# Kernel optimization log

Measured on AMD Instinct MI355X. Metric: run time of the kernel, lower is better.

The kernel has to match this reference:

```python
import jax, jax.numpy as jnp
import numpy as np
from jax import lax

B, C_IN, H, W = 4, 64, 128, 128
NUM_HIDDEN = 64
KSIZE = 3
DIST = 1
MOVES = 2 * DIST + 1          # 3
MOVESQ = MOVES * MOVES        # 9
TIME_STEPS = 8
LOSS_WEIGHT = 0.01


def _shift(a, dy, dx):
    """out(y, x) = a(y+dy, x+dx), zero outside; dy,dx in {-1,0,1}. a: [..., H, W]."""
    p = jnp.pad(a, [(0, 0)] * (a.ndim - 2) + [(1, 1), (1, 1)])
    h, w = a.shape[-2], a.shape[-1]
    return p[..., 1 + dy:1 + dy + h, 1 + dx:1 + dx + w]


def _gather(o4):
    # gather_kernel[i,0,i//3,i%3]=1 => channel i is o4 shifted by (i//3-1, i%3-1)
    return jnp.stack([_shift(o4, i // MOVES - 1, i % MOVES - 1) for i in range(MOVESQ)], axis=1)


def _merge(hxo):
    # hxo: [B, nh, 9, H, W]; merge_kernel[0, 9-i-1, i//3, i%3]=1 grouped per hidden channel
    # => merged(y,x) = sum_j hxo[:,:,j](y + 1 - j//3, x + 1 - j%3)
    return sum(_shift(hxo[:, :, j], 1 - j // MOVES, 1 - j % MOVES) for j in range(MOVESQ))


def _forward(x, mask, w_ih, b_ih, w_hh, b_hh, w_ho, b_ho):
    b, _, h, w = x.shape
    pad = KSIZE // 2
    i_all = lax.conv_general_dilated(
        x, w_ih, (1, 1), [(pad, pad), (pad, pad)],
        dimension_numbers=("NCHW", "OIHW", "NCHW")) + b_ih[None, :, None, None]
    i_r, i_i, i_n = jnp.split(i_all, 3, axis=1)

    h0 = jnp.zeros((b, NUM_HIDDEN, h, w), x.dtype)
    loss0 = jnp.zeros((b, MOVESQ, h, w), x.dtype)  # scalar init broadcasts to this shape

    def step(carry, _):
        hid, loss = carry
        hh = jnp.einsum("bchw,oc->bohw", hid, w_hh) + b_hh[None, :, None, None]
        h_r, h_i, h_n = jnp.split(hh, 3, axis=1)
        resetgate = jax.nn.sigmoid(i_r + h_r)
        inputgate = jax.nn.sigmoid(i_i + h_i)
        newgate = jnp.tanh(i_n + resetgate * h_n)
        hy = newgate + inputgate * (hid - newgate)
        o = jax.nn.softmax(jnp.einsum("bchw,oc->bohw", hy, w_ho) + b_ho[None, :, None, None], axis=1)
        o4 = o[:, 4]
        diff = (_gather(o4) - o) ** 2 * o
        bce = -jnp.mean(mask * jnp.log(1.0 - o4) + (1.0 - mask) * jnp.log(o4))
        loss = loss + bce + diff * LOSS_WEIGHT
        hxo = jnp.einsum("bchw,bdhw->bcdhw", hy, o)  # [B, nh, 9, H, W]
        h_next = _merge(hxo)
        return (h_next, loss), (h_next, o)

    (_, loss), (hiddens, outs) = lax.scan(step, (h0, loss0), None, length=TIME_STEPS)
    return hiddens, outs, loss


def setup_inputs() -> dict:
    key = jax.random.key(0)
    ks = jax.random.split(key, 8)
    s = 0.05
    return {
        "x": jax.random.normal(ks[0], (B, C_IN, H, W), jnp.float32),
        "mask": jax.random.uniform(ks[1], (B, H, W), jnp.float32),
        "w_ih": jax.random.normal(ks[2], (3 * NUM_HIDDEN, C_IN, KSIZE, KSIZE), jnp.float32) * s,
        "b_ih": jax.random.normal(ks[3], (3 * NUM_HIDDEN,), jnp.float32) * s,
        "w_hh": jax.random.normal(ks[4], (3 * NUM_HIDDEN, NUM_HIDDEN), jnp.float32) * s,
        "b_hh": jax.random.normal(ks[5], (3 * NUM_HIDDEN,), jnp.float32) * s,
        "w_ho": jax.random.normal(ks[6], (MOVESQ, NUM_HIDDEN), jnp.float32) * s,
        "b_ho": jax.random.normal(ks[7], (MOVESQ,), jnp.float32) * s,
    }


def reference(x, mask, w_ih, b_ih, w_hh, b_hh, w_ho, b_ho):
    return _forward(x, mask, w_ih, b_ih, w_hh, b_hh, w_ho, b_ho)
```

## Files before the change

### kernel.cpp

```cpp
#include <hip/hip_runtime.h>

#define NP 16384
#define HID_SZ 4194304
#define O_SZ   589824
#define OUTS_OFF 33554432
#define LOSS_OFF 38273024

#define WS_IALL0 0
#define WS_IALL1 4194304
#define WS_XTH   6291456
#define WS_HYA   8388608
#define WS_HYB   10485776
#define WS_WHH   12582944
#define WS_WHOB  12589088
#define WS_BTF   12589600
#define WS_BCEP  12644896

typedef __attribute__((ext_vector_type(8))) short bf16x8;
typedef __attribute__((ext_vector_type(8))) unsigned short ushort8;
typedef __attribute__((ext_vector_type(4))) unsigned short usht4;
typedef __attribute__((ext_vector_type(4))) float f32x4;

__device__ __forceinline__ float frcp(float x) { return __builtin_amdgcn_rcpf(x); }
__device__ __forceinline__ unsigned short f2bf(float f) {
    unsigned int u = __float_as_uint(f);
    return (unsigned short)((u + 0x7fffu + ((u >> 16) & 1u)) >> 16);
}
__device__ __forceinline__ float bf2f(unsigned short h) {
    return __uint_as_float(((unsigned int)h) << 16);
}
__device__ __forceinline__ int swz_bid(int bid) { return ((bid & 7) << 7) | (bid >> 3); }

__global__ __launch_bounds__(256) void prep_all(const float* __restrict__ x,
                                                const float* __restrict__ w_hh,
                                                const float* __restrict__ w_ho,
                                                const float* __restrict__ w_ih,
                                                unsigned short* __restrict__ xTh,
                                                unsigned short* __restrict__ whhBf,
                                                unsigned short* __restrict__ whoBf,
                                                unsigned short* __restrict__ BTf) {
    const int tid = threadIdx.x;
    if (blockIdx.x < 256) {
        const int p = blockIdx.x * 256 + tid;
        const int b = p >> 14, yx = p & 16383;
        const size_t base = ((size_t)p) << 6;
        for (int ic0 = 0; ic0 < 64; ic0 += 8) {
            ushort8 vh;
#pragma unroll
            for (int j = 0; j < 8; ++j)
                vh[j] = f2bf(x[(((size_t)(b * 64 + ic0 + j)) << 14) + yx]);
            *(ushort8*)(xTh + base + ic0) = vh;
        }
    } else {
        int i = (blockIdx.x - 256) * 256 + tid;
        if (i < 12288) {
            int f = i >> 9, r = i & 511;
            int lane = r >> 3, e = r & 7, lrow = lane & 15, lkq = lane >> 4;
            int ih = f / 12, n = f % 12;
            whhBf[i] = f2bf(w_hh[(n * 16 + lrow) * 64 + ih * 32 + lkq * 8 + e]);
        } else if (i < 13312) {
            int j = i - 12288;
            int f = j >> 9, r = j & 511;
            int lane = r >> 3, e = r & 7, lrow = lane & 15, lkq = lane >> 4;
            whoBf[j] = (lrow < 9) ? f2bf(w_ho[lrow * 64 + f * 32 + lkq * 8 + e]) : (unsigned short)0;
        } else if (i < 13312 + 110592) {
            int k2 = i - 13312;
            int f = k2 >> 9, r = k2 & 511;
            int lane = r >> 3, e = r & 7, lrow = lane & 15, lkq = lane >> 4;
            int tapih = f / 12, n = f % 12;
            int tap = tapih >> 1, ih = tapih & 1;
            int oc = n * 16 + lrow, ic = ih * 32 + lkq * 8 + e;
            BTf[k2] = f2bf(w_ih[(oc * 64 + ic) * 9 + tap]);
        }
    }
}

__global__ __launch_bounds__(256, 4) void conv_step0(const unsigned short* __restrict__ xTh,
                                                     const unsigned short* __restrict__ BTf,
                                                     const float* __restrict__ b_ih,
                                                     const float* __restrict__ b_hh,
                                                     const unsigned short* __restrict__ whoBf,
                                                     const float* __restrict__ b_ho,
                                                     const float* __restrict__ mask,
                                                     unsigned short* __restrict__ iall0,
                                                     unsigned short* __restrict__ iall1,
                                                     unsigned short* __restrict__ hy_cur,
                                                     float* __restrict__ o_out,
                                                     float* __restrict__ bceP) {
    __shared__ __align__(16) unsigned char smem[25344];
    unsigned short* hy_p = (unsigned short*)(smem + 10656);
    float* red = (float*)(smem + 19872);
    const int tid = threadIdx.x;
    const int bid = swz_bid(blockIdx.x);
    const int b = bid >> 8, y = (bid >> 1) & 127, hh2 = bid & 1;
    const int pxb = hh2 * 64, yxrow = y * 128;

    for (int ch = tid; ch < 1584; ch += 256) {
        const int row = ch / 528;
        const int rem = ch - row * 528;
        const int pxl = rem >> 3, icc = rem & 7;
        const int gy = y + row - 1, gx = pxb + pxl - 1;
        ushort8 vh = {};
        if (gy >= 0 && gy < 128 && gx >= 0 && gx < 128) {
            const size_t go = ((size_t)(b * 16384 + gy * 128 + gx)) * 64 + icc * 8;
            vh = *(const ushort8*)(xTh + go);
        }
        const int off = ((row * 66 + pxl) * 128 + icc * 16) ^ ((pxl & 7) << 4);
        *(ushort8*)(smem + off) = vh;
    }
    __syncthreads();

    const int lane = tid & 63, wv = tid >> 6;
    const int lrow = lane & 15, lkq = lane >> 4;
    const unsigned short* BTl = BTf + lane * 8;

    f32x4 acc[12] = {};
#pragma unroll
    for (int tap = 0; tap < 9; ++tap) {
        const int row = tap / 3, dx = tap % 3 - 1;
#pragma unroll
        for (int ih = 0; ih < 2; ++ih) {
            const int pxl = wv * 16 + lrow + dx + 1;
            const int off = ((row * 66 + pxl) * 128 + ih * 64 + lkq * 16) ^ ((pxl & 7) << 4);
            bf16x8 Ah = *(const bf16x8*)(smem + off);
#pragma unroll
            for (int n = 0; n < 12; ++n) {
                bf16x8 Bh = *(const bf16x8*)(BTl + (((tap * 2 + ih) * 12 + n) << 9));
                acc[n] = __builtin_amdgcn_mfma_f32_16x16x32_bf16(Ah, Bh, acc[n], 0, 0, 0);
            }
        }
    }

    float bias[12];
#pragma unroll
    for (int n = 0; n < 12; ++n) bias[n] = b_ih[n * 16 + lrow];
    const size_t rowb = (size_t)((b * 128 + y) * 2 + hh2);
    ushort8 v0[4];
    usht4 v1[4];
#pragma unroll
    for (int r = 0; r < 4; ++r) {
#pragma unroll
        for (int n = 0; n < 8; ++n) v0[r][n] = f2bf(acc[n][r] + bias[n]);
#pragma unroll
        for (int n = 8; n < 12; ++n) v1[r][n - 8] = f2bf(acc[n][r] + bias[n]);
        *(ushort8*)(iall0 + (rowb << 13) + ((wv * 4 + r) << 9) + lane * 8) = v0[r];
        *(usht4*)(iall1 + (rowb << 12) + ((wv * 4 + r) << 8) + lane * 4) = v1[r];
    }
    __syncthreads();

    float bhr[4], bhi[4], bhn[4];
#pragma unroll
    for (int nf = 0; nf < 4; ++nf) {
        bhr[nf] = b_hh[nf * 16 + lrow];
        bhi[nf] = b_hh[64 + nf * 16 + lrow];
        bhn[nf] = b_hh[128 + nf * 16 + lrow];
    }
#pragma unroll
    for (int nf = 0; nf < 4; ++nf) {
        const int g = nf * 16 + lrow;
        usht4 hv4;
#pragma unroll
        for (int rr = 0; rr < 4; ++rr) {
            const int pxl = wv * 16 + lkq * 4 + rr;
            float ir = bf2f(v0[rr][nf]), ii = bf2f(v0[rr][4 + nf]), inn = bf2f(v1[rr][nf]);
            float rg = frcp(1.0f + __expf(-(ir + bhr[nf])));
            float ig = frcp(1.0f + __expf(-(ii + bhi[nf])));
            float t2 = __expf(2.0f * (inn + rg * bhn[nf]));
            float nn = 1.0f - 2.0f * frcp(t2 + 1.0f);
            unsigned short hv = f2bf(nn + ig * (0.0f - nn));
            hy_p[pxl * 72 + g] = hv;
            hv4[rr] = hv;
        }
        *(usht4*)(hy_cur + (((size_t)(b * 64 + g)) << 14) + yxrow + pxb + wv * 16 + lkq * 4) = hv4;
    }
    __syncthreads();

    f32x4 aco = {};
#pragma unroll
    for (int ih = 0; ih < 2; ++ih) {
        const int pxa = wv * 16 + lrow;
        bf16x8 Ao = *(const bf16x8*)(hy_p + pxa * 72 + ih * 32 + lkq * 8);
        bf16x8 Bo = *(const bf16x8*)(whoBf + ((ih << 9) + lane * 8));
        aco = __builtin_amdgcn_mfma_f32_16x16x32_bf16(Ao, Bo, aco, 0, 0, 0);
    }
    const float bho = (lrow < 9) ? b_ho[lrow] : 0.0f;
    float ov[4];
    float vbce = 0.0f;
    const int yx0 = yxrow + pxb + wv * 16 + lkq * 4;
#pragma unroll
    for (int r = 0; r < 4; ++r) {
        float lg = aco[r] + bho;
        float v = (lrow < 9) ? lg : -1e30f;
        v = fmaxf(v, __shfl_xor(v, 1));
        v = fmaxf(v, __shfl_xor(v, 2));
        v = fmaxf(v, __shfl_xor(v, 4));
        v = fmaxf(v, __shfl_xor(v, 8));
        float e = (lrow < 9) ? __expf(lg - v) : 0.0f;
        float s = e;
        s += __shfl_xor(s, 1);
        s += __shfl_xor(s, 2);
        s += __shfl_xor(s, 4);
        s += __shfl_xor(s, 8);
        ov[r] = e * frcp(s);
    }
    if (lrow < 9) {
        f32x4 wvec = {ov[0], ov[1], ov[2], ov[3]};
        *(f32x4*)(o_out + (((size_t)(b * 9 + lrow)) << 14) + yx0) = wvec;
    }
    if (lrow == 4) {
        const f32x4 mk = *(const f32x4*)(mask + (((size_t)b) << 14) + yx0);
#pragma unroll
        for (int r = 0; r < 4; ++r)
            vbce += mk[r] * __logf(1.0f - ov[r]) + (1.0f - mk[r]) * __logf(ov[r]);
    }
    float v = (lrow == 4) ? vbce : 0.0f;
#pragma unroll
    for (int d = 1; d < 64; d <<= 1) v += __shfl_xor(v, d);
    if (lane == 0) red[wv] = v;
    __syncthreads();
    if (tid == 0) bceP[bid] = red[0] + red[1] + red[2] + red[3];
}

__global__ __launch_bounds__(256, 4) void step_kernel(const unsigned short* __restrict__ hyp,
                                                      const float* __restrict__ o_prev,
                                                      const unsigned short* __restrict__ iall0,
                                                      const unsigned short* __restrict__ iall1,
                                                      const unsigned short* __restrict__ whhBf,
                                                      const float* __restrict__ b_hh,
                                                      const unsigned short* __restrict__ whoBf,
                                                      const float* __restrict__ b_ho,
                                                      const float* __restrict__ mask,
                                                      float* __restrict__ hidd_out,
                                                      unsigned short* __restrict__ hy_cur,
                                                      float* __restrict__ o_out,
                                                      float* __restrict__ bceP) {
    __shared__ __align__(16) unsigned char smem[19904];
    float* ostrip = (float*)(smem + 8192);
    unsigned short* hy_p = (unsigned short*)(smem + 10656);
    float* red = (float*)(smem + 19872);

    const int tid = threadIdx.x;
    const int bid = swz_bid(blockIdx.x);
    const int b = bid >> 8, y = (bid >> 1) & 127, hh2 = bid & 1;
    const int pxb = hh2 * 64, yxrow = y * 128;

    {
        const int c = tid >> 2, pq = tid & 3;
        const int gx0 = pxb + pq * 16;
        const unsigned short* hb = hyp + (((size_t)(b * 64 + c)) << 14);
        ushort8 w8[3][4];
#pragma unroll
        for (int r = 0; r < 3; ++r) {
            const int gyc = min(max(y + r - 1, 0), 127);
            const unsigned short* src = hb + gyc * 128 + gx0 - 8;
#pragma unroll
            for (int q = 0; q < 4; ++q) w8[r][q] = *(const ushort8*)(src + q * 8);
        }
        const float* ob = o_prev + (((size_t)b * 9) << 14);
        for (int e = tid; e < 594; e += 256) {
            const int j = e / 66, s = e - j * 66;
            const int rj = y + 1 - j / 3;
            const int gx = pxb - 1 + s;
            const bool ok = (rj >= 0) && (rj < 128) && (gx >= 0) && (gx < 128);
            ostrip[j * 68 + s] = ok ? ob[(((size_t)j) << 14) + rj * 128 + gx] : 0.0f;
        }
        __syncthreads();

        float a[16];
#pragma unroll
        for (int px = 0; px < 16; ++px) a[px] = 0.0f;
#pragma unroll
        for (int r = 0; r < 3; ++r) {
            float wf[18];
#pragma unroll
            for (int k = 0; k < 18; ++k)
                wf[k] = bf2f((unsigned short)w8[r][(k + 7) >> 3][(k + 7) & 7]);
#pragma unroll
            for (int ex = -1; ex <= 1; ++ex) {
                const int idx = r * 3 + (ex + 1);
                const int j = 8 - idx;
                const float* osj = ostrip + j * 68 + pq * 16 + 1 + ex;
#pragma unroll
                for (int px = 0; px < 16; ++px)
                    a[px] = fmaf(wf[px + ex + 1], osj[px], a[px]);
            }
        }
        const size_t hob = (((size_t)(b * 64 + c)) << 14) + yxrow + gx0;
#pragma unroll
        for (int q = 0; q < 4; ++q) {
            f32x4 v = {a[q * 4], a[q * 4 + 1], a[q * 4 + 2], a[q * 4 + 3]};
            *(f32x4*)(hidd_out + hob + q * 4) = v;
        }
#pragma unroll
        for (int px = 0; px < 16; ++px) {
            const int pxl = pq * 16 + px;
            *(unsigned short*)(smem + ((pxl * 128 + c * 2) ^ ((pxl & 7) << 4))) = f2bf(a[px]);
        }
        __syncthreads();
    }

    const int lane = tid & 63, wv = tid >> 6;
    const int lrow = lane & 15, lkq = lane >> 4;

    f32x4 acc[12] = {};
    {
        bf16x8 Ah[2];
#pragma unroll
        for (int ih = 0; ih < 2; ++ih) {
            const int pxa = wv * 16 + lrow;
            const int off = (pxa * 128 + ih * 64 + lkq * 16) ^ ((pxa & 7) << 4);
            Ah[ih] = *(const bf16x8*)(smem + off);
        }
#pragma unroll
        for (int ih = 0; ih < 2; ++ih)
#pragma unroll
            for (int n = 0; n < 12; ++n) {
                bf16x8 Bh = *(const bf16x8*)(whhBf + (((ih * 12 + n) << 9) + lane * 8));
                acc[n] = __builtin_amdgcn_mfma_f32_16x16x32_bf16(Ah[ih], Bh, acc[n], 0, 0, 0);
            }
    }

    float bhr[4], bhi[4], bhn[4];
#pragma unroll
    for (int nf = 0; nf < 4; ++nf) {
        bhr[nf] = b_hh[nf * 16 + lrow];
        bhi[nf] = b_hh[64 + nf * 16 + lrow];
        bhn[nf] = b_hh[128 + nf * 16 + lrow];
    }
    const size_t rowb = (size_t)((b * 128 + y) * 2 + hh2);
    const unsigned short* p0 = iall0 + (rowb << 13) + (wv << 11) + lane * 8;
    const unsigned short* p1 = iall1 + (rowb << 12) + (wv << 10) + lane * 4;
    ushort8 lo[4];
    usht4 hi[4];
#pragma unroll
    for (int rr = 0; rr < 4; ++rr) {
        lo[rr] = *(const ushort8*)(p0 + (rr << 9));
        hi[rr] = *(const usht4*)(p1 + (rr << 8));
    }
#pragma unroll
    for (int nf = 0; nf < 4; ++nf) {
        const int g = nf * 16 + lrow;
        usht4 hv4;
#pragma unroll
        for (int rr = 0; rr < 4; ++rr) {
            const int pxl = wv * 16 + lkq * 4 + rr;
            float hr = bhr[nf] + acc[nf][rr];
            float hig = bhi[nf] + acc[nf + 4][rr];
            float hn = bhn[nf] + acc[nf + 8][rr];
            float ir = bf2f(lo[rr][nf]), ii = bf2f(lo[rr][4 + nf]), inn = bf2f(hi[rr][nf]);
            float rg = frcp(1.0f + __expf(-(ir + hr)));
            float ig = frcp(1.0f + __expf(-(ii + hig)));
            float t2 = __expf(2.0f * (inn + rg * hn));
            float nn = 1.0f - 2.0f * frcp(t2 + 1.0f);
            const int offA = (pxl * 128 + g * 2) ^ ((pxl & 7) << 4);
            float hp = bf2f(*(const unsigned short*)(smem + offA));
            unsigned short hv = f2bf(nn + ig * (hp - nn));
            hy_p[pxl * 72 + g] = hv;
            hv4[rr] = hv;
        }
        *(usht4*)(hy_cur + (((size_t)(b * 64 + g)) << 14) + yxrow + pxb + wv * 16 + lkq * 4) = hv4;
    }
    __syncthreads();

    f32x4 aco = {};
#pragma unroll
    for (int ih = 0; ih < 2; ++ih) {
        const int pxa = wv * 16 + lrow;
        bf16x8 Ao = *(const bf16x8*)(hy_p + pxa * 72 + ih * 32 + lkq * 8);
        bf16x8 Bo = *(const bf16x8*)(whoBf + ((ih << 9) + lane * 8));
        aco = __builtin_amdgcn_mfma_f32_16x16x32_bf16(Ao, Bo, aco, 0, 0, 0);
    }
    const float bho = (lrow < 9) ? b_ho[lrow] : 0.0f;
    float ov[4];
    float vbce = 0.0f;
    const int yx0 = yxrow + pxb + wv * 16 + lkq * 4;
#pragma unroll
    for (int r = 0; r < 4; ++r) {
        float lg = aco[r] + bho;
        float v = (lrow < 9) ? lg : -1e30f;
        v = fmaxf(v, __shfl_xor(v, 1));
        v = fmaxf(v, __shfl_xor(v, 2));
        v = fmaxf(v, __shfl_xor(v, 4));
        v = fmaxf(v, __shfl_xor(v, 8));
        float e = (lrow < 9) ? __expf(lg - v) : 0.0f;
        float s = e;
        s += __shfl_xor(s, 1);
        s += __shfl_xor(s, 2);
        s += __shfl_xor(s, 4);
        s += __shfl_xor(s, 8);
        ov[r] = e * frcp(s);
    }
    if (lrow < 9) {
        f32x4 wvec = {ov[0], ov[1], ov[2], ov[3]};
        *(f32x4*)(o_out + (((size_t)(b * 9 + lrow)) << 14) + yx0) = wvec;
    }
    if (lrow == 4) {
        const f32x4 mk = *(const f32x4*)(mask + (((size_t)b) << 14) + yx0);
#pragma unroll
        for (int r = 0; r < 4; ++r)
            vbce += mk[r] * __logf(1.0f - ov[r]) + (1.0f - mk[r]) * __logf(ov[r]);
    }
    float v = (lrow == 4) ? vbce : 0.0f;
#pragma unroll
    for (int d = 1; d < 64; d <<= 1) v += __shfl_xor(v, d);
    if (lane == 0) red[wv] = v;
    __syncthreads();
    if (tid == 0) bceP[bid] = red[0] + red[1] + red[2] + red[3];
}

__global__ __launch_bounds__(256) void final_fused(const unsigned short* __restrict__ hyp,
                                                   const float* __restrict__ o_all,
                                                   const float* __restrict__ bceP,
                                                   float* __restrict__ hidd7,
                                                   float* __restrict__ loss) {
    __shared__ __align__(16) float ostrip[9 * 68];
    __shared__ float o4s[3 * 68];
    __shared__ float redsh[256];
    const int tid = threadIdx.x;
    const int bid = swz_bid(blockIdx.x);
    const int b = bid >> 8, y = (bid >> 1) & 127, hh2 = bid & 1;
    const int pxb = hh2 * 64, yxrow = y * 128;

    float s = 0.0f;
    for (int i = tid; i < 8192; i += 256) s += bceP[i];
    redsh[tid] = s;
    __syncthreads();
    for (int off = 128; off > 0; off >>= 1) {
        if (tid < off) redsh[tid] += redsh[tid + off];
        __syncthreads();
    }
    const float bt = -redsh[0] * (1.0f / 65536.0f);

    {
        const int c = tid >> 2, pq = tid & 3;
        const int gx0 = pxb + pq * 16;
        const float* ob = o_all + (size_t)7 * O_SZ + (((size_t)b * 9) << 14);
        for (int e = tid; e < 594; e += 256) {
            const int j = e / 66, ss = e - j * 66;
            const int rj = y + 1 - j / 3;
            const int gx = pxb - 1 + ss;
            const bool ok = (rj >= 0) && (rj < 128) && (gx >= 0) && (gx < 128);
            ostrip[j * 68 + ss] = ok ? ob[(((size_t)j) << 14) + rj * 128 + gx] : 0.0f;
        }
        __syncthreads();
        const unsigned short* hb = hyp + (((size_t)(b * 64 + c)) << 14);
        float a[16];
#pragma unroll
        for (int px = 0; px < 16; ++px) a[px] = 0.0f;
#pragma unroll
        for (int r = 0; r < 3; ++r) {
            const int gyc = min(max(y + r - 1, 0), 127);
            const unsigned short* src = hb + gyc * 128 + gx0 - 8;
            ushort8 w8[4];
#pragma unroll
            for (int q = 0; q < 4; ++q) w8[q] = *(const ushort8*)(src + q * 8);
            float wf[18];
#pragma unroll
            for (int k = 0; k < 18; ++k)
                wf[k] = bf2f((unsigned short)w8[(k + 7) >> 3][(k + 7) & 7]);
#pragma unroll
            for (int ex = -1; ex <= 1; ++ex) {
                const int j = 8 - (r * 3 + (ex + 1));
                const float* osj = ostrip + j * 68 + pq * 16 + 1 + ex;
#pragma unroll
                for (int px = 0; px < 16; ++px)
                    a[px] = fmaf(wf[px + ex + 1], osj[px], a[px]);
            }
        }
        const size_t hob = (((size_t)(b * 64 + c)) << 14) + yxrow + gx0;
#pragma unroll
        for (int q = 0; q < 4; ++q) {
            f32x4 v = {a[q * 4], a[q * 4 + 1], a[q * 4 + 2], a[q * 4 + 3]};
            *(f32x4*)(hidd7 + hob + q * 4) = v;
        }
    }

    const int px = tid & 63, tq = tid >> 6;
    const int yx = yxrow + pxb + px;
    const int i0 = tq, i1 = tq + 4;
    float a0 = 0.0f, a1 = 0.0f, a2 = 0.0f;
    for (int t = 0; t < 8; ++t) {
        const float* ot = o_all + (size_t)t * O_SZ + (((size_t)b * 9) << 14);
        __syncthreads();
        for (int e = tid; e < 198; e += 256) {
            const int r = e / 66, ss = e - r * 66;
            const int ry = y + r - 1, gx = pxb - 1 + ss;
            const bool ok = (ry >= 0) && (ry < 128) && (gx >= 0) && (gx < 128);
            o4s[r * 68 + ss] = ok ? ot[(((size_t)4) << 14) + ry * 128 + gx] : 0.0f;
        }
        __syncthreads();
        {
            const float oi = ot[(((size_t)i0) << 14) + yx];
            const float g = o4s[(i0 / 3) * 68 + px + 1 + (i0 % 3 - 1)];
            const float d = g - oi;
            a0 = fmaf(d * d, oi, a0);
        }
        {
            const float oi = ot[(((size_t)i1) << 14) + yx];
            const float g = o4s[(i1 / 3) * 68 + px + 1 + (i1 % 3 - 1)];
            const float d = g - oi;
            a1 = fmaf(d * d, oi, a1);
        }
        if (tq == 0) {
            const float oi = ot[(((size_t)8) << 14) + yx];
            const float g = o4s[2 * 68 + px + 2];
            const float d = g - oi;
            a2 = fmaf(d * d, oi, a2);
        }
    }
    loss[(((size_t)(b * 9 + i0)) << 14) + yx] = a0 * 0.01f + bt;
    loss[(((size_t)(b * 9 + i1)) << 14) + yx] = a1 * 0.01f + bt;
    if (tq == 0) loss[(((size_t)(b * 9 + 8)) << 14) + yx] = a2 * 0.01f + bt;
}

extern "C" void kernel_launch(void* const* d_in, const int* in_sizes, int n_in,
                              void* d_out, int out_size, void* d_ws, size_t ws_size,
                              hipStream_t stream) {
    const float* x    = (const float*)d_in[0];
    const float* mask = (const float*)d_in[1];
    const float* w_ih = (const float*)d_in[2];
    const float* b_ih = (const float*)d_in[3];
    const float* w_hh = (const float*)d_in[4];
    const float* b_hh = (const float*)d_in[5];
    const float* w_ho = (const float*)d_in[6];
    const float* b_ho = (const float*)d_in[7];
    float* out = (float*)d_out;
    float* ws  = (float*)d_ws;

    unsigned short* iall0 = (unsigned short*)(ws + WS_IALL0);
    unsigned short* iall1 = (unsigned short*)(ws + WS_IALL1);
    unsigned short* xTh   = (unsigned short*)(ws + WS_XTH);
    unsigned short* hyA   = (unsigned short*)(ws + WS_HYA) + 8;
    unsigned short* hyB   = (unsigned short*)(ws + WS_HYB) + 8;
    unsigned short* whhBf = (unsigned short*)(ws + WS_WHH);
    unsigned short* whoBf = (unsigned short*)(ws + WS_WHOB);
    unsigned short* BTf   = (unsigned short*)(ws + WS_BTF);
    float* bceP = ws + WS_BCEP;
    float* lossp = out + LOSS_OFF;

    prep_all<<<740, 256, 0, stream>>>(x, w_hh, w_ho, w_ih, xTh, whhBf, whoBf, BTf);
    conv_step0<<<1024, 256, 0, stream>>>(xTh, BTf, b_ih, b_hh, whoBf, b_ho, mask,
                                         iall0, iall1, hyA, out + OUTS_OFF, bceP);
    for (int t = 1; t < 8; ++t) {
        const unsigned short* hypr = (t & 1) ? hyA : hyB;
        unsigned short* hyc = (t & 1) ? hyB : hyA;
        step_kernel<<<1024, 256, 0, stream>>>(hypr, out + OUTS_OFF + (size_t)(t - 1) * O_SZ,
                                              iall0, iall1, whhBf, b_hh, whoBf, b_ho, mask,
                                              out + (size_t)(t - 1) * HID_SZ, hyc,
                                              out + OUTS_OFF + (size_t)t * O_SZ,
                                              bceP + t * 1024);
    }
    final_fused<<<1024, 256, 0, stream>>>(hyB, out + OUTS_OFF, bceP,
                                          out + (size_t)7 * HID_SZ, lossp);
}
```

Measured before the change: 225.6 us.

## Retile step-0 conv MFMA as 2x6 per wave, hoist i_all loads, defer BCE reduction

The step-0 input convolution now gives each wave a 32-pixel by 96-channel tile (2 M-fragments by 6 N-fragments) instead of 16 pixels by all 192 channels. This lets each B-fragment load feed two MFMAs, roughly halving global weight reads. The results are repacked through shared memory to recover the original per-wave pixel layout for the gate math and the i_all stores, which adds extra barriers and LDS traffic. Separately, the recurrent step kernel issues its i_all global loads at kernel start so their latency overlaps the halo loads, and the final kernel moves its BCE block reduction after the hidden-state merge so the bceP loads overlap other work.

Measured after the change: 224.4 us. No clear change (-0.5%).

```diff
diff --git a/kernel.cpp b/kernel.cpp
--- a/kernel.cpp
+++ b/kernel.cpp
@@ -88,6 +88,8 @@
                                                      float* __restrict__ o_out,
                                                      float* __restrict__ bceP) {
     __shared__ __align__(16) unsigned char smem[25344];
+    unsigned short* ml0 = (unsigned short*)smem;
+    unsigned short* ml1 = (unsigned short*)(smem + 16384);
     unsigned short* hy_p = (unsigned short*)(smem + 10656);
     float* red = (float*)(smem + 19872);
     const int tid = threadIdx.x;
@@ -112,41 +114,70 @@
 
     const int lane = tid & 63, wv = tid >> 6;
     const int lrow = lane & 15, lkq = lane >> 4;
+    const int m2 = wv >> 1, nh = wv & 1;
     const unsigned short* BTl = BTf + lane * 8;
 
-    f32x4 acc[12] = {};
+    f32x4 acc[2][6] = {};
 #pragma unroll
     for (int tap = 0; tap < 9; ++tap) {
         const int row = tap / 3, dx = tap % 3 - 1;
 #pragma unroll
         for (int ih = 0; ih < 2; ++ih) {
-            const int pxl = wv * 16 + lrow + dx + 1;
-            const int off = ((row * 66 + pxl) * 128 + ih * 64 + lkq * 16) ^ ((pxl & 7) << 4);
-            bf16x8 Ah = *(const bf16x8*)(smem + off);
-#pragma unroll
-            for (int n = 0; n < 12; ++n) {
+            bf16x8 Ah[2];
+#pragma unroll
+            for (int mm = 0; mm < 2; ++mm) {
+                const int pxl = m2 * 32 + mm * 16 + lrow + dx + 1;
+                const int off = ((row * 66 + pxl) * 128 + ih * 64 + lkq * 16) ^ ((pxl & 7) << 4);
+                Ah[mm] = *(const bf16x8*)(smem + off);
+            }
+#pragma unroll
+            for (int nn = 0; nn < 6; ++nn) {
+                const int n = nh * 6 + nn;
                 bf16x8 Bh = *(const bf16x8*)(BTl + (((tap * 2 + ih) * 12 + n) << 9));
-                acc[n] = __builtin_amdgcn_mfma_f32_16x16x32_bf16(Ah, Bh, acc[n], 0, 0, 0);
+#pragma unroll
+                for (int mm = 0; mm < 2; ++mm)
+                    acc[mm][nn] = __builtin_amdgcn_mfma_f32_16x16x32_bf16(Ah[mm], Bh, acc[mm][nn], 0, 0, 0);
             }
         }
     }
-
-    float bias[12];
-#pragma unroll
-    for (int n = 0; n < 12; ++n) bias[n] = b_ih[n * 16 + lrow];
+    __syncthreads();
+
+    float bias[6];
+#pragma unroll
+    for (int nn = 0; nn < 6; ++nn) bias[nn] = b_ih[(nh * 6 + nn) * 16 + lrow];
+#pragma unroll
+    for (int mm = 0; mm < 2; ++mm) {
+        const int sbase = (m2 * 2 + mm) * 4;
+#pragma unroll
+        for (int r = 0; r < 4; ++r) {
+            const int s = sbase + r;
+#pragma unroll
+            for (int np = 0; np < 3; ++np) {
+                const int n = nh * 6 + np * 2;
+                unsigned int pk = (unsigned int)f2bf(acc[mm][np * 2][r] + bias[np * 2])
+                                | ((unsigned int)f2bf(acc[mm][np * 2 + 1][r] + bias[np * 2 + 1]) << 16);
+                if (n < 8) *(unsigned int*)(ml0 + s * 512 + lane * 8 + n) = pk;
+                else       *(unsigned int*)(ml1 + s * 256 + lane * 4 + (n - 8)) = pk;
+            }
+        }
+    }
+    __syncthreads();
+
+    ushort8 lo[4];
+    usht4 hi[4];
+#pragma unroll
+    for (int rr = 0; rr < 4; ++rr) {
+        lo[rr] = *(const ushort8*)(ml0 + ((wv * 4 + rr) << 9) + lane * 8);
+        hi[rr] = *(const usht4*)(ml1 + ((wv * 4 + rr) << 8) + lane * 4);
+    }
+    __syncthreads();
+
     const size_t rowb = (size_t)((b * 128 + y) * 2 + hh2);
-    ushort8 v0[4];
-    usht4 v1[4];
-#pragma unroll
-    for (int r = 0; r < 4; ++r) {
-#pragma unroll
-        for (int n = 0; n < 8; ++n) v0[r][n] = f2bf(acc[n][r] + bias[n]);
-#pragma unroll
-        for (int n = 8; n < 12; ++n) v1[r][n - 8] = f2bf(acc[n][r] + bias[n]);
-        *(ushort8*)(iall0 + (rowb << 13) + ((wv * 4 + r) << 9) + lane * 8) = v0[r];
-        *(usht4*)(iall1 + (rowb << 12) + ((wv * 4 + r) << 8) + lane * 4) = v1[r];
-    }
-    __syncthreads();
+#pragma unroll
+    for (int rr = 0; rr < 4; ++rr) {
+        *(ushort8*)(iall0 + (rowb << 13) + ((wv * 4 + rr) << 9) + lane * 8) = lo[rr];
+        *(usht4*)(iall1 + (rowb << 12) + ((wv * 4 + rr) << 8) + lane * 4) = hi[rr];
+    }
 
     float bhr[4], bhi[4], bhn[4];
 #pragma unroll
@@ -162,7 +193,7 @@
 #pragma unroll
         for (int rr = 0; rr < 4; ++rr) {
             const int pxl = wv * 16 + lkq * 4 + rr;
-            float ir = bf2f(v0[rr][nf]), ii = bf2f(v0[rr][4 + nf]), inn = bf2f(v1[rr][nf]);
+            float ir = bf2f(lo[rr][nf]), ii = bf2f(lo[rr][4 + nf]), inn = bf2f(hi[rr][nf]);
             float rg = frcp(1.0f + __expf(-(ir + bhr[nf])));
             float ig = frcp(1.0f + __expf(-(ii + bhi[nf])));
             float t2 = __expf(2.0f * (inn + rg * bhn[nf]));
@@ -243,6 +274,19 @@
     const int bid = swz_bid(blockIdx.x);
     const int b = bid >> 8, y = (bid >> 1) & 127, hh2 = bid & 1;
     const int pxb = hh2 * 64, yxrow = y * 128;
+    const int lane = tid & 63, wv = tid >> 6;
+    const int lrow = lane & 15, lkq = lane >> 4;
+
+    const size_t rowb = (size_t)((b * 128 + y) * 2 + hh2);
+    const unsigned short* p0 = iall0 + (rowb << 13) + (wv << 11) + lane * 8;
+    const unsigned short* p1 = iall1 + (rowb << 12) + (wv << 10) + lane * 4;
+    ushort8 lo[4];
+    usht4 hi[4];
+#pragma unroll
+    for (int rr = 0; rr < 4; ++rr) {
+        lo[rr] = *(const ushort8*)(p0 + (rr << 9));
+        hi[rr] = *(const usht4*)(p1 + (rr << 8));
+    }
 
     {
         const int c = tid >> 2, pq = tid & 3;
@@ -299,9 +343,6 @@
         __syncthreads();
     }
 
-    const int lane = tid & 63, wv = tid >> 6;
-    const int lrow = lane & 15, lkq = lane >> 4;
-
     f32x4 acc[12] = {};
     {
         bf16x8 Ah[2];
@@ -326,16 +367,6 @@
         bhr[nf] = b_hh[nf * 16 + lrow];
         bhi[nf] = b_hh[64 + nf * 16 + lrow];
         bhn[nf] = b_hh[128 + nf * 16 + lrow];
-    }
-    const size_t rowb = (size_t)((b * 128 + y) * 2 + hh2);
-    const unsigned short* p0 = iall0 + (rowb << 13) + (wv << 11) + lane * 8;
-    const unsigned short* p1 = iall1 + (rowb << 12) + (wv << 10) + lane * 4;
-    ushort8 lo[4];
-    usht4 hi[4];
-#pragma unroll
-    for (int rr = 0; rr < 4; ++rr) {
-        lo[rr] = *(const ushort8*)(p0 + (rr << 9));
-        hi[rr] = *(const usht4*)(p1 + (rr << 8));
     }
 #pragma unroll
     for (int nf = 0; nf < 4; ++nf) {
@@ -423,13 +454,6 @@
 
     float s = 0.0f;
     for (int i = tid; i < 8192; i += 256) s += bceP[i];
-    redsh[tid] = s;
-    __syncthreads();
-    for (int off = 128; off > 0; off >>= 1) {
-        if (tid < off) redsh[tid] += redsh[tid + off];
-        __syncthreads();
-    }
-    const float bt = -redsh[0] * (1.0f / 65536.0f);
 
     {
         const int c = tid >> 2, pq = tid & 3;
@@ -474,6 +498,15 @@
             *(f32x4*)(hidd7 + hob + q * 4) = v;
         }
     }
+
+    __syncthreads();
+    redsh[tid] = s;
+    __syncthreads();
+    for (int off = 128; off > 0; off >>= 1) {
+        if (tid < off) redsh[tid] += redsh[tid + off];
+        __syncthreads();
+    }
+    const float bt = -redsh[0] * (1.0f / 65536.0f);
 
     const int px = tid & 63, tq = tid >> 6;
     const int yx = yxrow + pxb + px;
```
